# Performance work log

Measured on AMD Instinct MI355X. Metric: run time of the kernel, lower is better.

The kernel has to match this reference:

```python
import jax, jax.numpy as jnp
import numpy as np

B = 2048        # batch of plans
N_LEAF = 1024   # scan nodes (leaves of complete binary tree)
F = 32          # node feature dim
H = 128         # neural-unit hidden dim
O = 32          # unit output dim = 1 (latency) + data_vec_dim (31)


def _mlp_params(key, in_dim, scale=0.05):
    k1, k2, k3 = jax.random.split(key, 3)
    return (
        jax.random.normal(k1, (in_dim, H), jnp.float32) * scale, jnp.zeros((H,), jnp.float32),
        jax.random.normal(k2, (H, H), jnp.float32) * scale, jnp.zeros((H,), jnp.float32),
        jax.random.normal(k3, (H, O), jnp.float32) * scale, jnp.zeros((O,), jnp.float32),
    )


def setup_inputs() -> dict:
    key = jax.random.key(0)
    k1, k2, k3, k4 = jax.random.split(key, 4)
    leaf_feats = jax.random.normal(k1, (B, N_LEAF, F), jnp.float32)
    # internal nodes stored level-by-level bottom-up: 512, 256, ..., 1  (total 1023)
    internal_feats = jax.random.normal(k2, (B, N_LEAF - 1, F), jnp.float32)
    sW1, sb1, sW2, sb2, sW3, sb3 = _mlp_params(k3, F)           # Scan unit (0 children)
    jW1, jb1, jW2, jb2, jW3, jb3 = _mlp_params(k4, F + 2 * O)   # Join unit (2 children)
    return dict(leaf_feats=leaf_feats, internal_feats=internal_feats,
                sW1=sW1, sb1=sb1, sW2=sW2, sb2=sb2, sW3=sW3, sb3=sb3,
                jW1=jW1, jb1=jb1, jW2=jW2, jb2=jb2, jW3=jW3, jb3=jb3)


def _unit(x, W1, b1, W2, b2, W3, b3):
    # Neural unit: 2 hidden ReLU layers -> O outputs (latency + data vector)
    h = jax.nn.relu(x @ W1 + b1)
    h = jax.nn.relu(h @ W2 + b2)
    return h @ W3 + b3


def reference(leaf_feats, internal_feats,
              sW1, sb1, sW2, sb2, sW3, sb3,
              jW1, jb1, jW2, jb2, jW3, jb3):
    # Leaves: Scan unit on node features alone
    cur = _unit(leaf_feats, sW1, sb1, sW2, sb2, sW3, sb3)  # [B, 1024, O]
    off, n = 0, N_LEAF // 2
    while n >= 1:  # static loop over tree levels (bottom-up)
        feats = internal_feats[:, off:off + n]             # [B, n, F]
        children = cur.reshape(B, n, 2 * O)                # concat of 2 child outputs
        x = jnp.concatenate([feats, children], axis=-1)    # [B, n, F + 2O]
        cur = _unit(x, jW1, jb1, jW2, jb2, jW3, jb3)       # [B, n, O]
        off += n
        n //= 2
    return cur[:, 0, 0]  # root latency (output[:, 0]) per plan -> [B]
```

## Files before the change

### kernel.cpp

```cpp
#include <hip/hip_runtime.h>
#include <hip/hip_bf16.h>


typedef _Float16 f16;
typedef _Float16 f16x8 __attribute__((ext_vector_type(8)));
typedef _Float16 f16x4 __attribute__((ext_vector_type(4)));
typedef float    f32x4 __attribute__((ext_vector_type(4)));

#define MFMA16(a, b, c) __builtin_amdgcn_mfma_f32_16x16x32_f16((a), (b), (c), 0, 0, 0)
#define LGKM0    asm volatile("s_waitcnt lgkmcnt(0)" ::: "memory")

#define OFF_S1 0
#define OFF_S2 4096
#define OFF_S3 20480
#define OFF_J1 24576
#define OFF_J2 36864
#define OFF_J3 53248
#define W_TOTAL 57344
#define CURA_BYTE_OFF 114688

__global__ void prep_weights(const float* __restrict__ sW1,
                             const float* __restrict__ sW2,
                             const float* __restrict__ sW3,
                             const float* __restrict__ jW1,
                             const float* __restrict__ jW2,
                             const float* __restrict__ jW3,
                             f16* __restrict__ wbuf)
{
    int idx = blockIdx.x * 256 + threadIdx.x;
    if (idx >= W_TOTAL) return;
    const float* W;
    int off, M, K;
    if (idx < OFF_S2)      { off = OFF_S1; M = 128; K = 32;  W = sW1; }
    else if (idx < OFF_S3) { off = OFF_S2; M = 128; K = 128; W = sW2; }
    else if (idx < OFF_J1) { off = OFF_S3; M = 32;  K = 128; W = sW3; }
    else if (idx < OFF_J2) { off = OFF_J1; M = 128; K = 96;  W = jW1; }
    else if (idx < OFF_J3) { off = OFF_J2; M = 128; K = 128; W = jW2; }
    else                   { off = OFF_J3; M = 32;  K = 128; W = jW3; }
    int r = idx - off;
    int m = r / K;
    int k = r - m * K;
    wbuf[idx] = (f16)W[(size_t)k * M + m];
}

__device__ __forceinline__ void gload16(const void* g, void* l)
{
    __builtin_amdgcn_global_load_lds(
        (const __attribute__((address_space(1))) void*)g,
        (__attribute__((address_space(3))) void*)l,
        16, 0, 0);
}

template <bool LEAF>
__global__ __launch_bounds__(256, LEAF ? 4 : 3)
void mlp_level(const float* __restrict__ feats,
               const f16*   __restrict__ cur_in,
               f16*         __restrict__ cur_out,
               const f16*   __restrict__ W1t,
               const f16*   __restrict__ W2t,
               const f16*   __restrict__ W3t,
               const float* __restrict__ b1,
               const float* __restrict__ b2,
               const float* __restrict__ b3,
               int rows, int log2n, int foff)
{
    constexpr int K1    = LEAF ? 32 : 96;
    constexpr int NK1   = LEAF ? 1 : 3;
    constexpr int PITCH = 136;

    __shared__ __align__(16) f16   h1[32 * PITCH];
    __shared__ __align__(16) f16   h2[32 * PITCH];
    __shared__ __align__(16) float fstage[2][32 * 32];
    __shared__ __align__(16) f16   cstage[(LEAF ? 1 : 2)][32 * 64];
    __shared__ __align__(16) float bias_lds[LEAF ? 288 : 1];

    const int tid  = threadIdx.x;
    const int wave = tid >> 6;
    const int lane = tid & 63;
    const int n    = lane & 15;
    const int q    = lane >> 4;
    const int n7   = n & 7;
    const int mrow = 32 * wave;
    const int l3g  = wave & 1;
    const int l3h  = wave >> 1;

    const int srow   = (wave << 3) + (lane >> 3);
    const int schunk = (lane & 7) ^ (lane >> 3);

    if constexpr (LEAF) {
        if (tid < 128) bias_lds[tid] = b1[tid];
        else           bias_lds[tid] = b2[tid - 128];
        if (tid < 32)  bias_lds[256 + tid] = b3[tid];
    }

    f16x8 A1[2][NK1], A2[2][4], A3[4];
#pragma unroll
    for (int mt = 0; mt < 2; ++mt)
#pragma unroll
        for (int ks = 0; ks < NK1; ++ks)
            A1[mt][ks] = *(const f16x8*)(W1t + (size_t)(mrow + 16 * mt + n) * K1 + 32 * ks + 8 * q);
#pragma unroll
    for (int mt = 0; mt < 2; ++mt)
#pragma unroll
        for (int ks = 0; ks < 4; ++ks)
            A2[mt][ks] = *(const f16x8*)(W2t + (size_t)(mrow + 16 * mt + n) * 128 + 32 * ks + 8 * q);
#pragma unroll
    for (int ks = 0; ks < 4; ++ks)
        A3[ks] = *(const f16x8*)(W3t + (size_t)(16 * l3h + n) * 128 + 32 * ks + 8 * q);

    f32x4 bf1[2], bf2[2], bf3;
    if constexpr (!LEAF) {
#pragma unroll
        for (int mt = 0; mt < 2; ++mt) {
            bf1[mt] = *(const f32x4*)(b1 + mrow + 16 * mt + 4 * q);
            bf2[mt] = *(const f32x4*)(b2 + mrow + 16 * mt + 4 * q);
        }
        bf3 = *(const f32x4*)(b3 + 16 * l3h + 4 * q);
    }

    auto stage = [&](int tg0, int sb) {
        int gr = tg0 + srow;
        const float* fsrc;
        if constexpr (LEAF) {
            fsrc = feats + (size_t)gr * 32 + schunk * 4;
        } else {
            int bb = gr >> log2n;
            int ii = gr & ((1 << log2n) - 1);
            fsrc = feats + ((size_t)bb * 1023 + foff + ii) * 32 + schunk * 4;
        }
        gload16(fsrc, &fstage[sb][wave * 256]);
        if constexpr (!LEAF)
            gload16(cur_in + (size_t)gr * 64 + schunk * 8, &cstage[sb][wave * 512]);
    };

    const int stride = gridDim.x * 32;
    int g0 = blockIdx.x * 32;
    if (g0 >= rows) return;

    int rb = 0;
    stage(g0, 0);
    LGKM0;

    for (; g0 < rows; g0 += stride) {
        int gnext = g0 + stride;
        stage(gnext < rows ? gnext : g0, rb ^ 1);

        if constexpr (LEAF) asm volatile("s_waitcnt vmcnt(1)" ::: "memory");
        else                asm volatile("s_waitcnt vmcnt(2)" ::: "memory");
        __builtin_amdgcn_s_barrier();

        f32x4 C[2][2];
#pragma unroll
        for (int g = 0; g < 2; ++g)
#pragma unroll
            for (int mt = 0; mt < 2; ++mt) {
                if constexpr (LEAF)
                    C[g][mt] = *(const f32x4*)&bias_lds[mrow + 16 * mt + 4 * q];
                else
                    C[g][mt] = bf1[mt];
            }

#pragma unroll
        for (int g = 0; g < 2; ++g) {
            const int r = 16 * g + n;
            f32x4 fa = *(const f32x4*)(&fstage[rb][r * 32 + (((2 * q)     ^ n7) * 4)]);
            f32x4 fb = *(const f32x4*)(&fstage[rb][r * 32 + (((2 * q + 1) ^ n7) * 4)]);
            f16x8 Bf;
#pragma unroll
            for (int j = 0; j < 4; ++j) {
                Bf[j]     = (f16)fa[j];
                Bf[4 + j] = (f16)fb[j];
            }
#pragma unroll
            for (int mt = 0; mt < 2; ++mt) C[g][mt] = MFMA16(A1[mt][0], Bf, C[g][mt]);
            if constexpr (!LEAF) {
                f16x8 cl = *(const f16x8*)(&cstage[rb][r * 64 + ((q       ^ n7) * 8)]);
                f16x8 cr = *(const f16x8*)(&cstage[rb][r * 64 + (((4 + q) ^ n7) * 8)]);
#pragma unroll
                for (int mt = 0; mt < 2; ++mt) C[g][mt] = MFMA16(A1[mt][1], cl, C[g][mt]);
#pragma unroll
                for (int mt = 0; mt < 2; ++mt) C[g][mt] = MFMA16(A1[mt][2], cr, C[g][mt]);
            }
        }
#pragma unroll
        for (int g = 0; g < 2; ++g)
#pragma unroll
            for (int mt = 0; mt < 2; ++mt) {
                f16x4 pk;
                pk[0] = (f16)fmaxf(C[g][mt][0], 0.0f);
                pk[1] = (f16)fmaxf(C[g][mt][1], 0.0f);
                pk[2] = (f16)fmaxf(C[g][mt][2], 0.0f);
                pk[3] = (f16)fmaxf(C[g][mt][3], 0.0f);
                *(f16x4*)(h1 + (16 * g + n) * PITCH + mrow + 16 * mt + 4 * q) = pk;
            }
        LGKM0;
        __builtin_amdgcn_s_barrier();

#pragma unroll
        for (int g = 0; g < 2; ++g)
#pragma unroll
            for (int mt = 0; mt < 2; ++mt) {
                if constexpr (LEAF)
                    C[g][mt] = *(const f32x4*)&bias_lds[128 + mrow + 16 * mt + 4 * q];
                else
                    C[g][mt] = bf2[mt];
            }
#pragma unroll
        for (int ks = 0; ks < 4; ++ks)
#pragma unroll
            for (int g = 0; g < 2; ++g) {
                f16x8 Bf = *(const f16x8*)(h1 + (16 * g + n) * PITCH + 32 * ks + 8 * q);
#pragma unroll
                for (int mt = 0; mt < 2; ++mt) C[g][mt] = MFMA16(A2[mt][ks], Bf, C[g][mt]);
            }
#pragma unroll
        for (int g = 0; g < 2; ++g)
#pragma unroll
            for (int mt = 0; mt < 2; ++mt) {
                f16x4 pk;
                pk[0] = (f16)fmaxf(C[g][mt][0], 0.0f);
                pk[1] = (f16)fmaxf(C[g][mt][1], 0.0f);
                pk[2] = (f16)fmaxf(C[g][mt][2], 0.0f);
                pk[3] = (f16)fmaxf(C[g][mt][3], 0.0f);
                *(f16x4*)(h2 + (16 * g + n) * PITCH + mrow + 16 * mt + 4 * q) = pk;
            }
        LGKM0;
        __builtin_amdgcn_s_barrier();

        f32x4 C3;
        if constexpr (LEAF) C3 = *(const f32x4*)&bias_lds[256 + 16 * l3h + 4 * q];
        else                C3 = bf3;
#pragma unroll
        for (int ks = 0; ks < 4; ++ks) {
            f16x8 Bf = *(const f16x8*)(h2 + (16 * l3g + n) * PITCH + 32 * ks + 8 * q);
            C3 = MFMA16(A3[ks], Bf, C3);
        }
        {
            f16x4 pk;
            pk[0] = (f16)C3[0]; pk[1] = (f16)C3[1]; pk[2] = (f16)C3[2]; pk[3] = (f16)C3[3];
            *(f16x4*)(cur_out + (size_t)(g0 + 16 * l3g + n) * 32 + 16 * l3h + 4 * q) = pk;
        }

        rb ^= 1;
    }
}

__global__ __launch_bounds__(256, 2)
void mlp_tail(const float* __restrict__ feats,
              const f16*   __restrict__ cur_in,
              float*       __restrict__ out_final,
              const f16*   __restrict__ W1t,
              const f16*   __restrict__ W2t,
              const f16*   __restrict__ W3t,
              const float* __restrict__ b1,
              const float* __restrict__ b2,
              const float* __restrict__ b3)
{
    __shared__ __align__(16) f16   h1[32 * 128];
    __shared__ __align__(16) f16   h2[32 * 128];
    __shared__ __align__(16) f16   cur_lds[32 * 32];
    __shared__ __align__(16) float bias_lds[288];

    const int tid  = threadIdx.x;
    const int wave = tid >> 6;
    const int lane = tid & 63;
    const int n    = lane & 15;
    const int q    = lane >> 4;
    const int n7   = n & 7;
    const int mrow = 32 * wave;
    const int l3g  = wave & 1;
    const int l3h  = wave >> 1;
    const int b0   = blockIdx.x * 2;

    if (tid < 128) bias_lds[tid] = b1[tid];
    else           bias_lds[tid] = b2[tid - 128];
    if (tid < 32)  bias_lds[256 + tid] = b3[tid];

    f16x8 A1[2][3], A2[2][4], A3[4];
#pragma unroll
    for (int mt = 0; mt < 2; ++mt)
#pragma unroll
        for (int ks = 0; ks < 3; ++ks)
            A1[mt][ks] = *(const f16x8*)(W1t + (size_t)(mrow + 16 * mt + n) * 96 + 32 * ks + 8 * q);
#pragma unroll
    for (int mt = 0; mt < 2; ++mt)
#pragma unroll
        for (int ks = 0; ks < 4; ++ks)
            A2[mt][ks] = *(const f16x8*)(W2t + (size_t)(mrow + 16 * mt + n) * 128 + 32 * ks + 8 * q);
#pragma unroll
    for (int ks = 0; ks < 4; ++ks)
        A3[ks] = *(const f16x8*)(W3t + (size_t)(16 * l3h + n) * 128 + 32 * ks + 8 * q);

    LGKM0; __builtin_amdgcn_s_barrier();

    int nlev = 16, lg = 4, fo = 992;
    for (int lev = 0; lev < 5; ++lev) {
        const int rows_t = 2 * nlev;
        f32x4 fa[2], fb[2];
        f16x8 cl[2], cr[2];
#pragma unroll
        for (int g = 0; g < 2; ++g) {
            int r   = 16 * g + n;
            int sel = (r >> lg) & 1;
            int i   = r & (nlev - 1);
            int rc  = sel * nlev + i;
            const float* frow = feats + ((size_t)(b0 + sel) * 1023 + fo + i) * 32;
            fa[g] = *(const f32x4*)(frow + 8 * q);
            fb[g] = *(const f32x4*)(frow + 8 * q + 4);
            if (lev == 0) {
                int gr = (b0 + sel) * 16 + i;
                cl[g] = *(const f16x8*)(cur_in + (size_t)(2 * gr) * 32 + 8 * q);
                cr[g] = *(const f16x8*)(cur_in + (size_t)(2 * gr) * 32 + 32 + 8 * q);
            } else {
                cl[g] = *(const f16x8*)&cur_lds[(2 * rc) * 32 + 8 * q];
                cr[g] = *(const f16x8*)&cur_lds[(2 * rc) * 32 + 32 + 8 * q];
            }
        }
        {
            f32x4 C[2][2];
#pragma unroll
            for (int mt = 0; mt < 2; ++mt) {
                f32x4 bv = *(const f32x4*)&bias_lds[mrow + 16 * mt + 4 * q];
                C[0][mt] = bv; C[1][mt] = bv;
            }
#pragma unroll
            for (int g = 0; g < 2; ++g) {
                f16x8 Bf;
#pragma unroll
                for (int j = 0; j < 4; ++j) { Bf[j] = (f16)fa[g][j]; Bf[4 + j] = (f16)fb[g][j]; }
#pragma unroll
                for (int mt = 0; mt < 2; ++mt) C[g][mt] = MFMA16(A1[mt][0], Bf, C[g][mt]);
#pragma unroll
                for (int mt = 0; mt < 2; ++mt) C[g][mt] = MFMA16(A1[mt][1], cl[g], C[g][mt]);
#pragma unroll
                for (int mt = 0; mt < 2; ++mt) C[g][mt] = MFMA16(A1[mt][2], cr[g], C[g][mt]);
            }
#pragma unroll
            for (int g = 0; g < 2; ++g)
#pragma unroll
                for (int mt = 0; mt < 2; ++mt) {
                    f16x4 pk;
                    pk[0] = (f16)fmaxf(C[g][mt][0], 0.0f);
                    pk[1] = (f16)fmaxf(C[g][mt][1], 0.0f);
                    pk[2] = (f16)fmaxf(C[g][mt][2], 0.0f);
                    pk[3] = (f16)fmaxf(C[g][mt][3], 0.0f);
                    const int ch = 4 * wave + 2 * mt + (q >> 1);
                    *(f16x4*)&h1[(16 * g + n) * 128 + ((ch ^ n7) << 3) + 4 * (q & 1)] = pk;
                }
        }
        LGKM0; __builtin_amdgcn_s_barrier();
        {
            f32x4 C[2][2];
#pragma unroll
            for (int mt = 0; mt < 2; ++mt) {
                f32x4 bv = *(const f32x4*)&bias_lds[128 + mrow + 16 * mt + 4 * q];
                C[0][mt] = bv; C[1][mt] = bv;
            }
#pragma unroll
            for (int ks = 0; ks < 4; ++ks)
#pragma unroll
                for (int g = 0; g < 2; ++g) {
                    f16x8 Bf = *(const f16x8*)&h1[(16 * g + n) * 128 + (((4 * ks + q) ^ n7) << 3)];
#pragma unroll
                    for (int mt = 0; mt < 2; ++mt) C[g][mt] = MFMA16(A2[mt][ks], Bf, C[g][mt]);
                }
#pragma unroll
            for (int g = 0; g < 2; ++g)
#pragma unroll
                for (int mt = 0; mt < 2; ++mt) {
                    f16x4 pk;
                    pk[0] = (f16)fmaxf(C[g][mt][0], 0.0f);
                    pk[1] = (f16)fmaxf(C[g][mt][1], 0.0f);
                    pk[2] = (f16)fmaxf(C[g][mt][2], 0.0f);
                    pk[3] = (f16)fmaxf(C[g][mt][3], 0.0f);
                    const int ch = 4 * wave + 2 * mt + (q >> 1);
                    *(f16x4*)&h2[(16 * g + n) * 128 + ((ch ^ n7) << 3) + 4 * (q & 1)] = pk;
                }
        }
        LGKM0; __builtin_amdgcn_s_barrier();
        {
            f32x4 C3 = *(const f32x4*)&bias_lds[256 + 16 * l3h + 4 * q];
#pragma unroll
            for (int ks = 0; ks < 4; ++ks) {
                f16x8 Bf = *(const f16x8*)&h2[(16 * l3g + n) * 128 + (((4 * ks + q) ^ n7) << 3)];
                C3 = MFMA16(A3[ks], Bf, C3);
            }
            if (nlev > 1) {
                int row = 16 * l3g + n;
                if (row < rows_t) {
                    f16x4 pk;
                    pk[0] = (f16)C3[0]; pk[1] = (f16)C3[1]; pk[2] = (f16)C3[2]; pk[3] = (f16)C3[3];
                    *(f16x4*)&cur_lds[row * 32 + 16 * l3h + 4 * q] = pk;
                }
            } else {
                if (l3g == 0 && l3h == 0 && q == 0 && n < 2)
                    out_final[b0 + n] = C3[0];
            }
        }
        LGKM0; __builtin_amdgcn_s_barrier();
        fo += nlev;
        nlev >>= 1;
        --lg;
    }
}

extern "C" void kernel_launch(void* const* d_in, const int* in_sizes, int n_in,
                              void* d_out, int out_size, void* d_ws, size_t ws_size,
                              hipStream_t stream)
{
    const float* leaf_feats     = (const float*)d_in[0];
    const float* internal_feats = (const float*)d_in[1];
    const float* sW1 = (const float*)d_in[2];  const float* sb1 = (const float*)d_in[3];
    const float* sW2 = (const float*)d_in[4];  const float* sb2 = (const float*)d_in[5];
    const float* sW3 = (const float*)d_in[6];  const float* sb3 = (const float*)d_in[7];
    const float* jW1 = (const float*)d_in[8];  const float* jb1 = (const float*)d_in[9];
    const float* jW2 = (const float*)d_in[10]; const float* jb2 = (const float*)d_in[11];
    const float* jW3 = (const float*)d_in[12]; const float* jb3 = (const float*)d_in[13];

    f16* wbuf = (f16*)d_ws;
    f16* curA = (f16*)((char*)d_ws + CURA_BYTE_OFF);
    f16* curB = (f16*)((char*)d_ws + CURA_BYTE_OFF + 134217728);

    prep_weights<<<(W_TOTAL + 255) / 256, 256, 0, stream>>>(
        sW1, sW2, sW3, jW1, jW2, jW3, wbuf);

    mlp_level<true><<<2048, 256, 0, stream>>>(
        leaf_feats, nullptr, curA,
        wbuf + OFF_S1, wbuf + OFF_S2, wbuf + OFF_S3,
        sb1, sb2, sb3,
        2048 * 1024, 0, 0);

    const f16* cin = curA;
    f16* cout = curB;
    int off = 0, lg = 9;
    for (int nlev = 512; nlev >= 32; nlev >>= 1, --lg) {
        int rows  = 2048 * nlev;
        int iters = rows / 32;
        int grid  = iters < 2048 ? iters : 2048;
        mlp_level<false><<<grid, 256, 0, stream>>>(
            internal_feats, cin, cout,
            wbuf + OFF_J1, wbuf + OFF_J2, wbuf + OFF_J3,
            jb1, jb2, jb3,
            rows, lg, off);
        off += nlev;
        f16* t = cout; cout = (f16*)cin; cin = t;
    }

    mlp_tail<<<1024, 256, 0, stream>>>(
        internal_feats, cin, (float*)d_out,
        wbuf + OFF_J1, wbuf + OFF_J2, wbuf + OFF_J3,
        jb1, jb2, jb3);
}
```

Measured before the change: 796.7 us.

## Split leaf kernel into 64-row tile variant with 2x2 wave layout and swizzled LDS

```diff
diff --git a/kernel.cpp b/kernel.cpp
--- a/kernel.cpp
+++ b/kernel.cpp
@@ -51,28 +51,174 @@
         16, 0, 0);
 }
 
-template <bool LEAF>
-__global__ __launch_bounds__(256, LEAF ? 4 : 3)
-void mlp_level(const float* __restrict__ feats,
-               const f16*   __restrict__ cur_in,
-               f16*         __restrict__ cur_out,
-               const f16*   __restrict__ W1t,
-               const f16*   __restrict__ W2t,
-               const f16*   __restrict__ W3t,
-               const float* __restrict__ b1,
-               const float* __restrict__ b2,
-               const float* __restrict__ b3,
-               int rows, int log2n, int foff)
+__global__ __launch_bounds__(256, 3)
+void mlp_leaf64(const float* __restrict__ feats,
+                f16*         __restrict__ cur_out,
+                const f16*   __restrict__ W1t,
+                const f16*   __restrict__ W2t,
+                const f16*   __restrict__ W3t,
+                const float* __restrict__ b1,
+                const float* __restrict__ b2,
+                const float* __restrict__ b3,
+                int nt)
 {
-    constexpr int K1    = LEAF ? 32 : 96;
-    constexpr int NK1   = LEAF ? 1 : 3;
+    __shared__ __align__(16) f16   h1[64 * 128];
+    __shared__ __align__(16) f16   h2[64 * 128];
+    __shared__ __align__(16) float fstage[2][64 * 32];
+    __shared__ __align__(16) float bias_lds[288];
+
+    const int tid  = threadIdx.x;
+    const int wave = tid >> 6;
+    const int lane = tid & 63;
+    const int n    = lane & 15;
+    const int q    = lane >> 4;
+    const int n7   = n & 7;
+    const int wm   = wave >> 1;
+    const int wn   = wave & 1;
+
+    const int schunk = (lane & 7) ^ (lane >> 3);
+
+    if (tid < 128) bias_lds[tid] = b1[tid];
+    else           bias_lds[tid] = b2[tid - 128];
+    if (tid < 32)  bias_lds[256 + tid] = b3[tid];
+
+    f16x8 A1[4], A2[4][4], A3[4];
+#pragma unroll
+    for (int mt = 0; mt < 4; ++mt)
+        A1[mt] = *(const f16x8*)(W1t + (size_t)(64 * wm + 16 * mt + n) * 32 + 8 * q);
+#pragma unroll
+    for (int mt = 0; mt < 4; ++mt)
+#pragma unroll
+        for (int ks = 0; ks < 4; ++ks)
+            A2[mt][ks] = *(const f16x8*)(W2t + (size_t)(64 * wm + 16 * mt + n) * 128 + 32 * ks + 8 * q);
+#pragma unroll
+    for (int ks = 0; ks < 4; ++ks)
+        A3[ks] = *(const f16x8*)(W3t + (size_t)(16 * wm + n) * 128 + 32 * ks + 8 * q);
+
+    auto stage = [&](int tg0, int sb) {
+#pragma unroll
+        for (int half = 0; half < 2; ++half) {
+            int gr = tg0 + 16 * wave + 8 * half + (lane >> 3);
+            gload16(feats + (size_t)gr * 32 + schunk * 4,
+                    &fstage[sb][wave * 512 + half * 256]);
+        }
+    };
+
+    const int stride = gridDim.x * 64;
+    int g0 = blockIdx.x * 64;
+    int rb = 0;
+    stage(g0, 0);
+    LGKM0;
+
+    for (int t = 0; t < nt; ++t, g0 += stride) {
+        stage(t + 1 < nt ? g0 + stride : g0, rb ^ 1);
+        asm volatile("s_waitcnt vmcnt(2)" ::: "memory");
+        __builtin_amdgcn_s_barrier();
+
+        f32x4 C[2][4];
+#pragma unroll
+        for (int mt = 0; mt < 4; ++mt) {
+            f32x4 bv = *(const f32x4*)&bias_lds[64 * wm + 16 * mt + 4 * q];
+            C[0][mt] = bv; C[1][mt] = bv;
+        }
+#pragma unroll
+        for (int g = 0; g < 2; ++g) {
+            const int r = 32 * wn + 16 * g + n;
+            f32x4 fa = *(const f32x4*)&fstage[rb][r * 32 + (((2 * q)     ^ n7) << 2)];
+            f32x4 fb = *(const f32x4*)&fstage[rb][r * 32 + (((2 * q + 1) ^ n7) << 2)];
+            f16x8 Bf;
+#pragma unroll
+            for (int j = 0; j < 4; ++j) { Bf[j] = (f16)fa[j]; Bf[4 + j] = (f16)fb[j]; }
+#pragma unroll
+            for (int mt = 0; mt < 4; ++mt) C[g][mt] = MFMA16(A1[mt], Bf, C[g][mt]);
+        }
+#pragma unroll
+        for (int g = 0; g < 2; ++g)
+#pragma unroll
+            for (int mt = 0; mt < 4; ++mt) {
+                f16x4 pk;
+                pk[0] = (f16)fmaxf(C[g][mt][0], 0.0f);
+                pk[1] = (f16)fmaxf(C[g][mt][1], 0.0f);
+                pk[2] = (f16)fmaxf(C[g][mt][2], 0.0f);
+                pk[3] = (f16)fmaxf(C[g][mt][3], 0.0f);
+                const int c = 8 * wm + 2 * mt + (q >> 1);
+                *(f16x4*)&h1[(32 * wn + 16 * g + n) * 128 + ((c ^ n7) << 3) + 4 * (q & 1)] = pk;
+            }
+        LGKM0;
+        __builtin_amdgcn_s_barrier();
+
+#pragma unroll
+        for (int mt = 0; mt < 4; ++mt) {
+            f32x4 bv = *(const f32x4*)&bias_lds[128 + 64 * wm + 16 * mt + 4 * q];
+            C[0][mt] = bv; C[1][mt] = bv;
+        }
+#pragma unroll
+        for (int ks = 0; ks < 4; ++ks)
+#pragma unroll
+            for (int g = 0; g < 2; ++g) {
+                const int r = 32 * wn + 16 * g + n;
+                f16x8 Bf = *(const f16x8*)&h1[r * 128 + (((4 * ks + q) ^ n7) << 3)];
+#pragma unroll
+                for (int mt = 0; mt < 4; ++mt) C[g][mt] = MFMA16(A2[mt][ks], Bf, C[g][mt]);
+            }
+#pragma unroll
+        for (int g = 0; g < 2; ++g)
+#pragma unroll
+            for (int mt = 0; mt < 4; ++mt) {
+                f16x4 pk;
+                pk[0] = (f16)fmaxf(C[g][mt][0], 0.0f);
+                pk[1] = (f16)fmaxf(C[g][mt][1], 0.0f);
+                pk[2] = (f16)fmaxf(C[g][mt][2], 0.0f);
+                pk[3] = (f16)fmaxf(C[g][mt][3], 0.0f);
+                const int c = 8 * wm + 2 * mt + (q >> 1);
+                *(f16x4*)&h2[(32 * wn + 16 * g + n) * 128 + ((c ^ n7) << 3) + 4 * (q & 1)] = pk;
+            }
+        LGKM0;
+        __builtin_amdgcn_s_barrier();
+
+        f32x4 C3[2];
+        {
+            f32x4 bv = *(const f32x4*)&bias_lds[256 + 16 * wm + 4 * q];
+            C3[0] = bv; C3[1] = bv;
+        }
+#pragma unroll
+        for (int g = 0; g < 2; ++g)
+#pragma unroll
+            for (int ks = 0; ks < 4; ++ks) {
+                const int r = 32 * wn + 16 * g + n;
+                f16x8 Bf = *(const f16x8*)&h2[r * 128 + (((4 * ks + q) ^ n7) << 3)];
+                C3[g] = MFMA16(A3[ks], Bf, C3[g]);
+            }
+#pragma unroll
+        for (int g = 0; g < 2; ++g) {
+            f16x4 pk;
+            pk[0] = (f16)C3[g][0]; pk[1] = (f16)C3[g][1];
+            pk[2] = (f16)C3[g][2]; pk[3] = (f16)C3[g][3];
+            *(f16x4*)(cur_out + (size_t)(g0 + 32 * wn + 16 * g + n) * 32 + 16 * wm + 4 * q) = pk;
+        }
+        rb ^= 1;
+    }
+}
+
+__global__ __launch_bounds__(256, 3)
+void mlp_join(const float* __restrict__ feats,
+              const f16*   __restrict__ cur_in,
+              f16*         __restrict__ cur_out,
+              const f16*   __restrict__ W1t,
+              const f16*   __restrict__ W2t,
+              const f16*   __restrict__ W3t,
+              const float* __restrict__ b1,
+              const float* __restrict__ b2,
+              const float* __restrict__ b3,
+              int rows, int log2n, int foff)
+{
+    constexpr int K1    = 96;
     constexpr int PITCH = 136;
 
     __shared__ __align__(16) f16   h1[32 * PITCH];
     __shared__ __align__(16) f16   h2[32 * PITCH];
     __shared__ __align__(16) float fstage[2][32 * 32];
-    __shared__ __align__(16) f16   cstage[(LEAF ? 1 : 2)][32 * 64];
-    __shared__ __align__(16) float bias_lds[LEAF ? 288 : 1];
+    __shared__ __align__(16) f16   cstage[2][32 * 64];
 
     const int tid  = threadIdx.x;
     const int wave = tid >> 6;
@@ -87,17 +233,11 @@
     const int srow   = (wave << 3) + (lane >> 3);
     const int schunk = (lane & 7) ^ (lane >> 3);
 
-    if constexpr (LEAF) {
-        if (tid < 128) bias_lds[tid] = b1[tid];
-        else           bias_lds[tid] = b2[tid - 128];
-        if (tid < 32)  bias_lds[256 + tid] = b3[tid];
-    }
-
-    f16x8 A1[2][NK1], A2[2][4], A3[4];
+    f16x8 A1[2][3], A2[2][4], A3[4];
 #pragma unroll
     for (int mt = 0; mt < 2; ++mt)
 #pragma unroll
-        for (int ks = 0; ks < NK1; ++ks)
+        for (int ks = 0; ks < 3; ++ks)
             A1[mt][ks] = *(const f16x8*)(W1t + (size_t)(mrow + 16 * mt + n) * K1 + 32 * ks + 8 * q);
 #pragma unroll
     for (int mt = 0; mt < 2; ++mt)
@@ -109,28 +249,20 @@
         A3[ks] = *(const f16x8*)(W3t + (size_t)(16 * l3h + n) * 128 + 32 * ks + 8 * q);
 
     f32x4 bf1[2], bf2[2], bf3;
-    if constexpr (!LEAF) {
-#pragma unroll
-        for (int mt = 0; mt < 2; ++mt) {
-            bf1[mt] = *(const f32x4*)(b1 + mrow + 16 * mt + 4 * q);
-            bf2[mt] = *(const f32x4*)(b2 + mrow + 16 * mt + 4 * q);
-        }
-        bf3 = *(const f32x4*)(b3 + 16 * l3h + 4 * q);
+#pragma unroll
+    for (int mt = 0; mt < 2; ++mt) {
+        bf1[mt] = *(const f32x4*)(b1 + mrow + 16 * mt + 4 * q);
+        bf2[mt] = *(const f32x4*)(b2 + mrow + 16 * mt + 4 * q);
     }
+    bf3 = *(const f32x4*)(b3 + 16 * l3h + 4 * q);
 
     auto stage = [&](int tg0, int sb) {
         int gr = tg0 + srow;
-        const float* fsrc;
-        if constexpr (LEAF) {
-            fsrc = feats + (size_t)gr * 32 + schunk * 4;
-        } else {
-            int bb = gr >> log2n;
-            int ii = gr & ((1 << log2n) - 1);
-            fsrc = feats + ((size_t)bb * 1023 + foff + ii) * 32 + schunk * 4;
-        }
+        int bb = gr >> log2n;
+        int ii = gr & ((1 << log2n) - 1);
+        const float* fsrc = feats + ((size_t)bb * 1023 + foff + ii) * 32 + schunk * 4;
         gload16(fsrc, &fstage[sb][wave * 256]);
-        if constexpr (!LEAF)
-            gload16(cur_in + (size_t)gr * 64 + schunk * 8, &cstage[sb][wave * 512]);
+        gload16(cur_in + (size_t)gr * 64 + schunk * 8, &cstage[sb][wave * 512]);
     };
 
     const int stride = gridDim.x * 32;
@@ -139,26 +271,19 @@
 
     int rb = 0;
     stage(g0, 0);
-    LGKM0;
 
     for (; g0 < rows; g0 += stride) {
         int gnext = g0 + stride;
         stage(gnext < rows ? gnext : g0, rb ^ 1);
 
-        if constexpr (LEAF) asm volatile("s_waitcnt vmcnt(1)" ::: "memory");
-        else                asm volatile("s_waitcnt vmcnt(2)" ::: "memory");
+        asm volatile("s_waitcnt vmcnt(2)" ::: "memory");
         __builtin_amdgcn_s_barrier();
 
         f32x4 C[2][2];
 #pragma unroll
         for (int g = 0; g < 2; ++g)
 #pragma unroll
-            for (int mt = 0; mt < 2; ++mt) {
-                if constexpr (LEAF)
-                    C[g][mt] = *(const f32x4*)&bias_lds[mrow + 16 * mt + 4 * q];
-                else
-                    C[g][mt] = bf1[mt];
-            }
+            for (int mt = 0; mt < 2; ++mt) C[g][mt] = bf1[mt];
 
 #pragma unroll
         for (int g = 0; g < 2; ++g) {
@@ -167,20 +292,15 @@
             f32x4 fb = *(const f32x4*)(&fstage[rb][r * 32 + (((2 * q + 1) ^ n7) * 4)]);
             f16x8 Bf;
 #pragma unroll
-            for (int j = 0; j < 4; ++j) {
-                Bf[j]     = (f16)fa[j];
-                Bf[4 + j] = (f16)fb[j];
-            }
+            for (int j = 0; j < 4; ++j) { Bf[j] = (f16)fa[j]; Bf[4 + j] = (f16)fb[j]; }
 #pragma unroll
             for (int mt = 0; mt < 2; ++mt) C[g][mt] = MFMA16(A1[mt][0], Bf, C[g][mt]);
-            if constexpr (!LEAF) {
-                f16x8 cl = *(const f16x8*)(&cstage[rb][r * 64 + ((q       ^ n7) * 8)]);
-                f16x8 cr = *(const f16x8*)(&cstage[rb][r * 64 + (((4 + q) ^ n7) * 8)]);
-#pragma unroll
-                for (int mt = 0; mt < 2; ++mt) C[g][mt] = MFMA16(A1[mt][1], cl, C[g][mt]);
-#pragma unroll
-                for (int mt = 0; mt < 2; ++mt) C[g][mt] = MFMA16(A1[mt][2], cr, C[g][mt]);
-            }
+            f16x8 cl = *(const f16x8*)(&cstage[rb][r * 64 + ((q       ^ n7) * 8)]);
+            f16x8 cr = *(const f16x8*)(&cstage[rb][r * 64 + (((4 + q) ^ n7) * 8)]);
+#pragma unroll
+            for (int mt = 0; mt < 2; ++mt) C[g][mt] = MFMA16(A1[mt][1], cl, C[g][mt]);
+#pragma unroll
+            for (int mt = 0; mt < 2; ++mt) C[g][mt] = MFMA16(A1[mt][2], cr, C[g][mt]);
         }
 #pragma unroll
         for (int g = 0; g < 2; ++g)
@@ -199,12 +319,7 @@
 #pragma unroll
         for (int g = 0; g < 2; ++g)
 #pragma unroll
-            for (int mt = 0; mt < 2; ++mt) {
-                if constexpr (LEAF)
-                    C[g][mt] = *(const f32x4*)&bias_lds[128 + mrow + 16 * mt + 4 * q];
-                else
-                    C[g][mt] = bf2[mt];
-            }
+            for (int mt = 0; mt < 2; ++mt) C[g][mt] = bf2[mt];
 #pragma unroll
         for (int ks = 0; ks < 4; ++ks)
 #pragma unroll
@@ -227,9 +342,7 @@
         LGKM0;
         __builtin_amdgcn_s_barrier();
 
-        f32x4 C3;
-        if constexpr (LEAF) C3 = *(const f32x4*)&bias_lds[256 + 16 * l3h + 4 * q];
-        else                C3 = bf3;
+        f32x4 C3 = bf3;
 #pragma unroll
         for (int ks = 0; ks < 4; ++ks) {
             f16x8 Bf = *(const f16x8*)(h2 + (16 * l3g + n) * PITCH + 32 * ks + 8 * q);
@@ -240,7 +353,6 @@
             pk[0] = (f16)C3[0]; pk[1] = (f16)C3[1]; pk[2] = (f16)C3[2]; pk[3] = (f16)C3[3];
             *(f16x4*)(cur_out + (size_t)(g0 + 16 * l3g + n) * 32 + 16 * l3h + 4 * q) = pk;
         }
-
         rb ^= 1;
     }
 }
@@ -424,11 +536,11 @@
     prep_weights<<<(W_TOTAL + 255) / 256, 256, 0, stream>>>(
         sW1, sW2, sW3, jW1, jW2, jW3, wbuf);
 
-    mlp_level<true><<<2048, 256, 0, stream>>>(
-        leaf_feats, nullptr, curA,
+    mlp_leaf64<<<2048, 256, 0, stream>>>(
+        leaf_feats, curA,
         wbuf + OFF_S1, wbuf + OFF_S2, wbuf + OFF_S3,
         sb1, sb2, sb3,
-        2048 * 1024, 0, 0);
+        16);
 
     const f16* cin = curA;
     f16* cout = curB;
@@ -437,7 +549,7 @@
         int rows  = 2048 * nlev;
         int iters = rows / 32;
         int grid  = iters < 2048 ? iters : 2048;
-        mlp_level<false><<<grid, 256, 0, stream>>>(
+        mlp_join<<<grid, 256, 0, stream>>>(
             internal_feats, cin, cout,
             wbuf + OFF_J1, wbuf + OFF_J2, wbuf + OFF_J3,
             jb1, jb2, jb3,
```

Result: slower. 883.1 us (+10.9%).
